# Kernel optimization log

Hardware: AMD Instinct MI355X
Metric: run time of the kernel (lower is better)

The kernel has to match this reference:

```python
import jax, jax.numpy as jnp
import numpy as np

B, N, D = 8, 4096, 256   # batch, nodes, input = hidden = output dim
TD, GD, L = 64, 73, 2    # topo_dim, gdv_dim, num_passes
NEG = -1e9               # fp32 mask value from get_mask_value


def setup_inputs() -> dict:
    key = jax.random.key(0)
    ks = jax.random.split(key, 24)
    s = 0.05
    nrm = lambda k, shp: jax.random.normal(k, shp, jnp.float32) * s
    d = {}
    d['x'] = jax.random.normal(ks[0], (B, N, D), jnp.float32)
    d['adj'] = jax.random.randint(ks[1], (D, D), 0, 2, jnp.int32)
    d['gdv'] = jax.random.uniform(ks[2], (D, GD), dtype=jnp.float32)
    d['W_in'] = nrm(ks[3], (D, D));   d['b_in'] = nrm(ks[4], (D,))
    d['W_out'] = nrm(ks[5], (D, D)); d['b_out'] = nrm(ks[6], (D,))
    d['g1_W'] = nrm(ks[7], (GD, TD));  d['g1_b'] = nrm(ks[8], (TD,))
    d['g2_W'] = nrm(ks[9], (TD, TD));  d['g2_b'] = nrm(ks[10], (TD,))
    d['gres_W'] = nrm(ks[11], (GD, TD)); d['gres_b'] = nrm(ks[12], (TD,))
    d['ln_g'] = jnp.ones((D,), jnp.float32); d['ln_b'] = jnp.zeros((D,), jnp.float32)
    d['Wf'] = nrm(ks[13], (L, D, D)); d['bf'] = nrm(ks[14], (L, D))
    d['Wt'] = nrm(ks[15], (L, TD, D)); d['bt'] = nrm(ks[16], (L, D))
    d['wa_feat'] = nrm(ks[17], (L, 2 * D)); d['ba_feat'] = nrm(ks[18], (L,))
    d['wa_topo'] = nrm(ks[19], (L, 2 * D)); d['ba_topo'] = nrm(ks[20], (L,))
    d['Wo'] = nrm(ks[21], (L, D, D)); d['bo'] = nrm(ks[22], (L, D))
    d['lng'] = jnp.ones((L, D), jnp.float32); d['lnb'] = jnp.zeros((L, D), jnp.float32)
    return d


def _ln(x, g, b, eps=1e-5):
    m = x.mean(-1, keepdims=True)
    v = ((x - m) ** 2).mean(-1, keepdims=True)
    return (x - m) * jax.lax.rsqrt(v + eps) * g + b


def reference(x, adj, gdv, W_in, b_in, W_out, b_out, g1_W, g1_b, g2_W, g2_b,
              gres_W, gres_b, ln_g, ln_b, Wf, bf, Wt, bt, wa_feat, ba_feat,
              wa_topo, ba_topo, Wo, bo, lng, lnb):
    # GDV -> topo embedding; batch-independent, so keep it [D, TD] instead of
    # the original's broadcast [B, D, TD] (same math, no duplicated compute).
    g = gdv / (gdv.sum(1, keepdims=True) + 1e-6)
    t = jax.nn.relu(g @ g1_W + g1_b) @ g2_W + g2_b + (g @ gres_W + gres_b)  # [D, TD]
    mask = adj == 0  # [D, D]
    h = x @ W_in + b_in  # [B, N, D]
    for l in range(L):
        Tp = t @ Wt[l] + bt[l]  # [D, D] topo projection (hidden_dim == D)
        # topo_attn Linear(2D,1) on cat([T_i, T_j]) == (Tp@w_i)_i + (Tp@w_j)_j + bias
        wi, wj = wa_topo[l, :D], wa_topo[l, D:]
        e_topo = jax.nn.leaky_relu((Tp @ wi)[:, None] + (Tp @ wj)[None, :] + ba_topo[l])
        beta = jax.nn.softmax(jnp.where(mask, NEG, e_topo), axis=-1)  # [D, D]
        T_out = beta @ Tp  # [D, D]
        Hp = h @ Wf[l] + bf[l]  # [B, N, D]
        # feature_attn Linear(2D,1) on cat([H_n, T_f]) decomposed the same way
        wh, wt = wa_feat[l, :D], wa_feat[l, D:]
        e_feat = jax.nn.leaky_relu((Hp @ wh)[:, :, None] + (T_out @ wt)[None, None, :] + ba_feat[l])
        alpha = jax.nn.softmax(e_feat, axis=-1)  # [B, N, D]
        h_new = jnp.einsum('bnf,fh->bnh', alpha, T_out)
        # output proj + residual (input==output -> plain add), dropout = identity (eval)
        h = _ln(h_new @ Wo[l] + bo[l] + h, lng[l], lnb[l])
    return _ln(h @ W_out + b_out, ln_g, ln_b)
```

## Files before the change

### kernel.cpp

```cpp
#include <hip/hip_runtime.h>
#include <hip/hip_bf16.h>


typedef float f32x4 __attribute__((ext_vector_type(4)));
typedef short bf16x8 __attribute__((ext_vector_type(8)));

__device__ __forceinline__ unsigned short f2bf(float f) {
  unsigned int u = __builtin_bit_cast(unsigned int, f);
  u += 0x7FFFu + ((u >> 16) & 1u);
  return (unsigned short)(u >> 16);
}
__device__ __forceinline__ float bf2f(unsigned short u) {
  return __builtin_bit_cast(float, (unsigned int)u << 16);
}
__device__ __forceinline__ float lrelu(float x) { return x > 0.f ? x : 0.01f * x; }

template <int CTRL>
__device__ __forceinline__ float dpp_ror_add(float v) {
  int s = __builtin_amdgcn_update_dpp(0, __builtin_bit_cast(int, v), CTRL, 0xf, 0xf, true);
  return v + __builtin_bit_cast(float, s);
}
__device__ __forceinline__ float sum16(float v) {
  v = dpp_ror_add<0x128>(v);
  v = dpp_ror_add<0x124>(v);
  v = dpp_ror_add<0x122>(v);
  v = dpp_ror_add<0x121>(v);
  return v;
}

__device__ __forceinline__ float block_sum(float v, float* s4, int t) {
  v = sum16(v);
  v += __shfl_xor(v, 16, 64);
  v += __shfl_xor(v, 32, 64);
  __syncthreads();
  if ((t & 63) == 0) s4[t >> 6] = v;
  __syncthreads();
  return s4[0] + s4[1] + s4[2] + s4[3];
}
__device__ __forceinline__ float block_max(float v, float* s4, int t) {
#pragma unroll
  for (int m = 1; m < 64; m <<= 1) v = fmaxf(v, __shfl_xor(v, m, 64));
  __syncthreads();
  if ((t & 63) == 0) s4[t >> 6] = v;
  __syncthreads();
  return fmaxf(fmaxf(s4[0], s4[1]), fmaxf(s4[2], s4[3]));
}

__device__ __forceinline__ int swz_off(int k, int n) {
  return ((((k >> 5) * 16 + (n >> 4)) * 4 + ((k >> 3) & 3)) * 16 + (n & 15)) * 8 + (k & 7);
}
__device__ __forceinline__ int alds_byte(int n, int m) {
  int grp = n >> 3;
  int base = (grp * 32 + m) * 16 + (n & 7) * 2;
  return base ^ ((grp & 7) << 4);
}

__global__ void ta_kernel(const float* __restrict__ gdv,
                          const float* __restrict__ g1W, const float* __restrict__ g1b,
                          const float* __restrict__ g2W, const float* __restrict__ g2b,
                          const float* __restrict__ grW, const float* __restrict__ grb,
                          const float* __restrict__ Wt, const float* __restrict__ bt,
                          const float* __restrict__ wat,
                          float* __restrict__ Tp, float* __restrict__ pb, float* __restrict__ qb) {
  int l = blockIdx.x >> 8, i = blockIdx.x & 255, t = threadIdx.x;
  __shared__ float gs[73], as_[64], ts[64], s4[4];
  float gv = (t < 73) ? gdv[i * 73 + t] : 0.f;
  float gsum = block_sum(gv, s4, t);
  if (t < 73) gs[t] = gv / (gsum + 1e-6f);
  __syncthreads();
  if (t < 64) {
    float a = g1b[t], gr = grb[t];
    for (int k = 0; k < 73; ++k) { float gk = gs[k]; a = fmaf(gk, g1W[k * 64 + t], a); gr = fmaf(gk, grW[k * 64 + t], gr); }
    as_[t] = fmaxf(a, 0.f);
    ts[t] = gr + g2b[t];
  }
  __syncthreads();
  float tv = 0.f;
  if (t < 64) {
    tv = ts[t];
    for (int k = 0; k < 64; ++k) tv = fmaf(as_[k], g2W[k * 64 + t], tv);
  }
  __syncthreads();
  if (t < 64) ts[t] = tv;
  __syncthreads();
  float tp = bt[l * 256 + t];
  for (int k = 0; k < 64; ++k) tp = fmaf(ts[k], Wt[(l * 64 + k) * 256 + t], tp);
  Tp[(l * 256 + i) * 256 + t] = tp;
  float pp = block_sum(tp * wat[l * 512 + t], s4, t);
  float qq = block_sum(tp * wat[l * 512 + 256 + t], s4, t);
  if (t == 0) { pb[l * 256 + i] = pp; qb[l * 256 + i] = qq; }
}

__global__ void tb_kernel(const int* __restrict__ adj, const float* __restrict__ Tp,
                          const float* __restrict__ pb, const float* __restrict__ qb,
                          const float* __restrict__ batopo, const float* __restrict__ Wo,
                          const float* __restrict__ wafeat, const float* __restrict__ bafeat,
                          const float* __restrict__ Wf, const float* __restrict__ bfv,
                          const float* __restrict__ Win, const float* __restrict__ Wout,
                          float* __restrict__ rp, float* __restrict__ ub, float* __restrict__ cb,
                          unsigned short* __restrict__ Uws) {
  int b = blockIdx.x, t = threadIdx.x;
  if (b >= 512) {
    int bb = b - 512;
    const float* src = (bb < 16) ? Win : Wout;
    unsigned short* dst = Uws + ((bb < 16) ? 0 : 65536);
    int r0 = (bb & 15) * 16;
    for (int kk = 0; kk < 16; ++kk) {
      int k = r0 + kk;
      dst[swz_off(k, t)] = f2bf(src[k * 256 + t]);
    }
    return;
  }
  int l = b >> 8, i = b & 255;
  __shared__ float beta[256], tout[256], s4[4];
  float e = pb[l * 256 + i] + qb[l * 256 + t] + batopo[l];
  e = lrelu(e);
  if (adj[i * 256 + t] == 0) e = -1e9f;
  float mx = block_max(e, s4, t);
  float w = __expf(e - mx);
  float Z = block_sum(w, s4, t);
  beta[t] = w / Z;
  __syncthreads();
  float acc = 0.f;
  for (int j = 0; j < 256; ++j) acc = fmaf(beta[j], Tp[(l * 256 + j) * 256 + t], acc);
  tout[t] = acc;
  __syncthreads();
  const float* WoL = Wo + l * 65536;
  float macc = 0.f;
  for (int h2 = 0; h2 < 256; ++h2) macc = fmaf(tout[h2], WoL[h2 * 256 + t], macc);
  Uws[131072 + l * 65536 + swz_off(i, t)] = f2bf(macc);
  const float* wf = wafeat + l * 512;
  float rsum = block_sum(tout[t] * wf[256 + t], s4, t);
  if (t == 0) rp[l * 256 + i] = rsum + bafeat[l];
  float usum = block_sum(Wf[(l * 256 + i) * 256 + t] * wf[t], s4, t);
  if (t == 0) ub[l * 256 + i] = usum;
  if (i == 0) {
    float csum = block_sum(bfv[l * 256 + t] * wf[t], s4, t);
    if (t == 0) cb[l] = csum;
  }
}

#define MFMA(A, B, C) __builtin_amdgcn_mfma_f32_16x16x32_bf16(A, B, C, 0, 0, 0)

__device__ __forceinline__ void kloop(const char* smc, const unsigned short* Bws,
                                      int wid, int lane, int li, int g, f32x4 acc[2][2]) {
  const bf16x8* Bw = (const bf16x8*)Bws + wid * 2 * 64 + lane;
  bf16x8 b0 = Bw[0], b1 = Bw[64];
#pragma unroll
  for (int kb = 0; kb < 8; ++kb) {
    bf16x8 nb0, nb1;
    if (kb < 7) {
      nb0 = Bw[(kb + 1) * 1024];
      nb1 = Bw[(kb + 1) * 1024 + 64];
    }
    int grp = kb * 4 + g;
    int ab = ((grp * 32 + li) * 16) ^ ((grp & 7) << 4);
    bf16x8 a0 = *(const bf16x8*)(smc + ab);
    bf16x8 a1 = *(const bf16x8*)(smc + ab + 256);
    acc[0][0] = MFMA(a0, b0, acc[0][0]);
    acc[1][0] = MFMA(a1, b0, acc[1][0]);
    acc[0][1] = MFMA(a0, b1, acc[0][1]);
    acc[1][1] = MFMA(a1, b1, acc[1][1]);
    if (kb < 7) { b0 = nb0; b1 = nb1; }
  }
}

#define S_REDUCE(UBARR, CBV)                                                   \
  {                                                                            \
    float u0_ = UBARR[ncol[0]], u1_ = UBARR[ncol[1]];                          \
    _Pragma("unroll") for (int rt = 0; rt < 2; ++rt) {                         \
      float sp[4];                                                             \
      _Pragma("unroll") for (int r = 0; r < 4; ++r)                            \
        sp[r] = h[rt][0][r] * u0_ + h[rt][1][r] * u1_;                         \
      _Pragma("unroll") for (int r = 0; r < 4; ++r) sp[r] = sum16(sp[r]);      \
      if (li == 0) {                                                           \
        _Pragma("unroll") for (int r = 0; r < 4; ++r)                          \
          red[wid][rt * 16 + g * 4 + r] = sp[r];                               \
      }                                                                        \
    }                                                                          \
    __syncthreads();                                                           \
    if (t < 32) {                                                              \
      float S = 0.f;                                                           \
      _Pragma("unroll") for (int w = 0; w < 8; ++w) S += red[w][t];            \
      row_s[t] = S + (CBV);                                                    \
    }                                                                          \
    __syncthreads();                                                           \
  }

#define LN_STATS()                                                             \
  {                                                                            \
    _Pragma("unroll") for (int rt = 0; rt < 2; ++rt) {                         \
      float sA[4], sQ[4];                                                      \
      _Pragma("unroll") for (int r = 0; r < 4; ++r) {                          \
        float a0 = h[rt][0][r], a1 = h[rt][1][r];                              \
        sA[r] = a0 + a1;                                                       \
        sQ[r] = a0 * a0 + a1 * a1;                                             \
      }                                                                        \
      _Pragma("unroll") for (int r = 0; r < 4; ++r) {                          \
        sA[r] = sum16(sA[r]); sQ[r] = sum16(sQ[r]);                            \
      }                                                                        \
      if (li == 0) {                                                           \
        _Pragma("unroll") for (int r = 0; r < 4; ++r) {                        \
          int row_ = rt * 16 + g * 4 + r;                                      \
          red[wid][row_] = sA[r]; red[8 + wid][row_] = sQ[r];                  \
        }                                                                      \
      }                                                                        \
    }                                                                          \
    __syncthreads();                                                           \
    if (t < 32) {                                                              \
      float S = 0.f, Q = 0.f;                                                  \
      _Pragma("unroll") for (int w = 0; w < 8; ++w) { S += red[w][t]; Q += red[8 + w][t]; } \
      float mean_ = S * (1.f / 256.f);                                         \
      float var_ = Q * (1.f / 256.f) - mean_ * mean_;                          \
      mr_s[t][0] = mean_; mr_s[t][1] = rsqrtf(var_ + 1e-5f);                   \
    }                                                                          \
    __syncthreads();                                                           \
  }

__global__ __launch_bounds__(512) void fused_kernel(
    const float* __restrict__ x,
    const float* __restrict__ rp, const float* __restrict__ ub, const float* __restrict__ cbp,
    const unsigned short* __restrict__ Uws,
    const float* __restrict__ bin, const float* __restrict__ bo,
    const float* __restrict__ lng, const float* __restrict__ lnb,
    const float* __restrict__ bout, const float* __restrict__ lngf, const float* __restrict__ lnbf,
    float* __restrict__ out) {
  __shared__ unsigned short alds[8192];
  __shared__ float c_bin[256], c_bout[256], c_lngf[256], c_lnbf[256];
  __shared__ float c_ub[2][256], c_bo[2][256], c_lng[2][256], c_lnb[2][256], c_rp[2][256];
  __shared__ float red[16][32];
  __shared__ float row_s[32], invz_s[32];
  __shared__ float mr_s[32][2];
  __shared__ float scal_s[4];
  char* smc = (char*)alds;

  const int wg = blockIdx.x, t = threadIdx.x;
  const int wid = t >> 6, lane = t & 63, li = lane & 15, g = lane >> 4;
  const int rowbase = wg * 32;
  int ncol[2]; ncol[0] = wid * 32 + li; ncol[1] = wid * 32 + 16 + li;

  if (t < 256) {
    c_bin[t] = bin[t]; c_ub[0][t] = ub[t]; c_bo[0][t] = bo[t];
    c_lng[0][t] = lng[t]; c_lnb[0][t] = lnb[t]; c_rp[0][t] = rp[t];
  } else {
    int u = t - 256;
    c_bout[u] = bout[u]; c_lngf[u] = lngf[u]; c_lnbf[u] = lnbf[u];
    c_ub[1][u] = ub[256 + u]; c_bo[1][u] = bo[256 + u];
    c_lng[1][u] = lng[256 + u]; c_lnb[1][u] = lnb[256 + u]; c_rp[1][u] = rp[256 + u];
  }
  if (t == 0) { scal_s[2] = cbp[0]; scal_s[3] = cbp[1]; }

#pragma unroll
  for (int it = 0; it < 4; ++it) {
    int flat = it * 2048 + t * 4;
    int m = flat >> 8, col = flat & 255;
    const float4 xv = *(const float4*)(x + (rowbase + m) * 256 + col);
    ushort4 pk; pk.x = f2bf(xv.x); pk.y = f2bf(xv.y); pk.z = f2bf(xv.z); pk.w = f2bf(xv.w);
    *(ushort4*)(smc + alds_byte(col, m)) = pk;
  }
  __syncthreads();
  if (wid < 2) {
    float m2 = fmaxf(fmaxf(c_rp[wid][lane], c_rp[wid][lane + 64]),
                     fmaxf(c_rp[wid][lane + 128], c_rp[wid][lane + 192]));
#pragma unroll
    for (int mm = 1; mm < 64; mm <<= 1) m2 = fmaxf(m2, __shfl_xor(m2, mm, 64));
    if (lane == 0) scal_s[wid] = m2;
  }

  float h[2][2][4];

  {
    f32x4 acc[2][2];
#pragma unroll
    for (int a = 0; a < 2; ++a)
#pragma unroll
      for (int c = 0; c < 2; ++c) { f32x4 z = {0.f, 0.f, 0.f, 0.f}; acc[a][c] = z; }
    kloop(smc, Uws, wid, lane, li, g, acc);
#pragma unroll
    for (int rt = 0; rt < 2; ++rt)
#pragma unroll
      for (int ct = 0; ct < 2; ++ct)
#pragma unroll
        for (int r = 0; r < 4; ++r) h[rt][ct][r] = acc[rt][ct][r] + c_bin[ncol[ct]];
    S_REDUCE(c_ub[0], scal_s[2]);
  }

#pragma unroll 1
  for (int l = 0; l < 2; ++l) {
    {
      int row = t & 31, p = t >> 5;
      float sm = row_s[row];
      float mx = lrelu(sm + scal_s[l]);
      float z = 0.f;
#pragma unroll
      for (int j = 0; j < 2; ++j) {
        int grp = p * 2 + j;
        float w0 = __expf(lrelu(sm + c_rp[l][grp * 8 + 0]) - mx);
        float w1 = __expf(lrelu(sm + c_rp[l][grp * 8 + 1]) - mx);
        float w2 = __expf(lrelu(sm + c_rp[l][grp * 8 + 2]) - mx);
        float w3 = __expf(lrelu(sm + c_rp[l][grp * 8 + 3]) - mx);
        float w4 = __expf(lrelu(sm + c_rp[l][grp * 8 + 4]) - mx);
        float w5 = __expf(lrelu(sm + c_rp[l][grp * 8 + 5]) - mx);
        float w6 = __expf(lrelu(sm + c_rp[l][grp * 8 + 6]) - mx);
        float w7 = __expf(lrelu(sm + c_rp[l][grp * 8 + 7]) - mx);
        unsigned short u0 = f2bf(w0), u1 = f2bf(w1), u2 = f2bf(w2), u3 = f2bf(w3);
        unsigned short u4 = f2bf(w4), u5 = f2bf(w5), u6 = f2bf(w6), u7 = f2bf(w7);
        z += bf2f(u0) + bf2f(u1) + bf2f(u2) + bf2f(u3) +
             bf2f(u4) + bf2f(u5) + bf2f(u6) + bf2f(u7);
        uint4 pk;
        pk.x = (unsigned int)u0 | ((unsigned int)u1 << 16);
        pk.y = (unsigned int)u2 | ((unsigned int)u3 << 16);
        pk.z = (unsigned int)u4 | ((unsigned int)u5 << 16);
        pk.w = (unsigned int)u6 | ((unsigned int)u7 << 16);
        int byte = ((grp * 32 + row) * 16) ^ ((grp & 7) << 4);
        *(uint4*)(smc + byte) = pk;
      }
      red[p][row] = z;
    }
    __syncthreads();
    if (t < 32) {
      float Z = 0.f;
#pragma unroll
      for (int p = 0; p < 16; ++p) Z += red[p][t];
      invz_s[t] = 1.f / Z;
    }
    __syncthreads();

    f32x4 acc[2][2];
#pragma unroll
    for (int a = 0; a < 2; ++a)
#pragma unroll
      for (int c = 0; c < 2; ++c) { f32x4 z = {0.f, 0.f, 0.f, 0.f}; acc[a][c] = z; }
    kloop(smc, Uws + 131072 + l * 65536, wid, lane, li, g, acc);

#pragma unroll
    for (int rt = 0; rt < 2; ++rt)
#pragma unroll
      for (int r = 0; r < 4; ++r) {
        int row = rt * 16 + g * 4 + r;
        float iz = invz_s[row];
#pragma unroll
        for (int ct = 0; ct < 2; ++ct)
          h[rt][ct][r] = fmaf(acc[rt][ct][r], iz, c_bo[l][ncol[ct]] + h[rt][ct][r]);
      }
    LN_STATS();
#pragma unroll
    for (int rt = 0; rt < 2; ++rt)
#pragma unroll
      for (int r = 0; r < 4; ++r) {
        int row = rt * 16 + g * 4 + r;
        float mean = mr_s[row][0], rstd = mr_s[row][1];
#pragma unroll
        for (int ct = 0; ct < 2; ++ct)
          h[rt][ct][r] = (h[rt][ct][r] - mean) * rstd * c_lng[l][ncol[ct]] + c_lnb[l][ncol[ct]];
      }
    if (l == 0) S_REDUCE(c_ub[1], scal_s[3]);
  }

#pragma unroll
  for (int rt = 0; rt < 2; ++rt)
#pragma unroll
    for (int ct = 0; ct < 2; ++ct)
#pragma unroll
      for (int r = 0; r < 4; ++r) {
        int row = rt * 16 + g * 4 + r;
        *(unsigned short*)(smc + alds_byte(ncol[ct], row)) = f2bf(h[rt][ct][r]);
      }
  __syncthreads();
  {
    f32x4 acc[2][2];
#pragma unroll
    for (int a = 0; a < 2; ++a)
#pragma unroll
      for (int c = 0; c < 2; ++c) { f32x4 z = {0.f, 0.f, 0.f, 0.f}; acc[a][c] = z; }
    kloop(smc, Uws + 65536, wid, lane, li, g, acc);
#pragma unroll
    for (int rt = 0; rt < 2; ++rt)
#pragma unroll
      for (int ct = 0; ct < 2; ++ct)
#pragma unroll
        for (int r = 0; r < 4; ++r) h[rt][ct][r] = acc[rt][ct][r] + c_bout[ncol[ct]];
    LN_STATS();
#pragma unroll
    for (int rt = 0; rt < 2; ++rt)
#pragma unroll
      for (int r = 0; r < 4; ++r) {
        int row = rt * 16 + g * 4 + r;
        float mean = mr_s[row][0], rstd = mr_s[row][1];
#pragma unroll
        for (int ct = 0; ct < 2; ++ct)
          out[(rowbase + row) * 256 + ncol[ct]] =
              (h[rt][ct][r] - mean) * rstd * c_lngf[ncol[ct]] + c_lnbf[ncol[ct]];
      }
  }
}

extern "C" void kernel_launch(void* const* d_in, const int* in_sizes, int n_in,
                              void* d_out, int out_size, void* d_ws, size_t ws_size,
                              hipStream_t stream) {
  const float* x    = (const float*)d_in[0];
  const int*   adj  = (const int*)d_in[1];
  const float* gdv  = (const float*)d_in[2];
  const float* Win  = (const float*)d_in[3];
  const float* bin  = (const float*)d_in[4];
  const float* Wout = (const float*)d_in[5];
  const float* bout = (const float*)d_in[6];
  const float* g1W  = (const float*)d_in[7];
  const float* g1b  = (const float*)d_in[8];
  const float* g2W  = (const float*)d_in[9];
  const float* g2b  = (const float*)d_in[10];
  const float* grW  = (const float*)d_in[11];
  const float* grb  = (const float*)d_in[12];
  const float* lngf = (const float*)d_in[13];
  const float* lnbf = (const float*)d_in[14];
  const float* Wf   = (const float*)d_in[15];
  const float* bfv  = (const float*)d_in[16];
  const float* Wt   = (const float*)d_in[17];
  const float* bt   = (const float*)d_in[18];
  const float* waf  = (const float*)d_in[19];
  const float* baf  = (const float*)d_in[20];
  const float* wat  = (const float*)d_in[21];
  const float* bat  = (const float*)d_in[22];
  const float* Wo   = (const float*)d_in[23];
  const float* bo   = (const float*)d_in[24];
  const float* lng  = (const float*)d_in[25];
  const float* lnb  = (const float*)d_in[26];
  float* out = (float*)d_out;

  float* W = (float*)d_ws;
  float* Tp = W;
  float* pb = W + 131072;
  float* qb = W + 131584;
  float* rp = W + 132096;
  float* ub = W + 132608;
  float* cb = W + 133120;
  unsigned short* Uws = (unsigned short*)(W + 133184);

  ta_kernel<<<512, 256, 0, stream>>>(gdv, g1W, g1b, g2W, g2b, grW, grb, Wt, bt, wat, Tp, pb, qb);
  tb_kernel<<<544, 256, 0, stream>>>(adj, Tp, pb, qb, bat, Wo, waf, baf, Wf, bfv, Win, Wout, rp, ub, cb, Uws);
  fused_kernel<<<1024, 512, 0, stream>>>(x, rp, ub, cb, Uws, bin, bo, lng, lnb, bout, lngf, lnbf, out);
}
```

Measured before the change: 75.45 us.

## Deepen B-operand prefetch, raise MFMA priority, stagger workgroup start, nontemporal I/O

```diff
diff --git a/kernel.cpp b/kernel.cpp
--- a/kernel.cpp
+++ b/kernel.cpp
@@ -145,23 +145,27 @@
 __device__ __forceinline__ void kloop(const char* smc, const unsigned short* Bws,
                                       int wid, int lane, int li, int g, f32x4 acc[2][2]) {
   const bf16x8* Bw = (const bf16x8*)Bws + wid * 2 * 64 + lane;
-  bf16x8 b0 = Bw[0], b1 = Bw[64];
+  bf16x8 b0a = Bw[0], b1a = Bw[64];
+  bf16x8 b0b = Bw[1024], b1b = Bw[1024 + 64];
 #pragma unroll
   for (int kb = 0; kb < 8; ++kb) {
     bf16x8 nb0, nb1;
-    if (kb < 7) {
-      nb0 = Bw[(kb + 1) * 1024];
-      nb1 = Bw[(kb + 1) * 1024 + 64];
+    if (kb < 6) {
+      nb0 = Bw[(kb + 2) * 1024];
+      nb1 = Bw[(kb + 2) * 1024 + 64];
     }
     int grp = kb * 4 + g;
     int ab = ((grp * 32 + li) * 16) ^ ((grp & 7) << 4);
     bf16x8 a0 = *(const bf16x8*)(smc + ab);
     bf16x8 a1 = *(const bf16x8*)(smc + ab + 256);
-    acc[0][0] = MFMA(a0, b0, acc[0][0]);
-    acc[1][0] = MFMA(a1, b0, acc[1][0]);
-    acc[0][1] = MFMA(a0, b1, acc[0][1]);
-    acc[1][1] = MFMA(a1, b1, acc[1][1]);
-    if (kb < 7) { b0 = nb0; b1 = nb1; }
+    __builtin_amdgcn_s_setprio(1);
+    acc[0][0] = MFMA(a0, b0a, acc[0][0]);
+    acc[1][0] = MFMA(a1, b0a, acc[1][0]);
+    acc[0][1] = MFMA(a0, b1a, acc[0][1]);
+    acc[1][1] = MFMA(a1, b1a, acc[1][1]);
+    __builtin_amdgcn_s_setprio(0);
+    b0a = b0b; b1a = b1b;
+    if (kb < 6) { b0b = nb0; b1b = nb1; }
   }
 }
 
@@ -239,6 +243,13 @@
   const int rowbase = wg * 32;
   int ncol[2]; ncol[0] = wid * 32 + li; ncol[1] = wid * 32 + 16 + li;
 
+  {
+    int ph = wg & 3;
+    if (ph > 0) __builtin_amdgcn_s_sleep(24);
+    if (ph > 1) __builtin_amdgcn_s_sleep(24);
+    if (ph > 2) __builtin_amdgcn_s_sleep(24);
+  }
+
   if (t < 256) {
     c_bin[t] = bin[t]; c_ub[0][t] = ub[t]; c_bo[0][t] = bo[t];
     c_lng[0][t] = lng[t]; c_lnb[0][t] = lnb[t]; c_rp[0][t] = rp[t];
@@ -254,7 +265,7 @@
   for (int it = 0; it < 4; ++it) {
     int flat = it * 2048 + t * 4;
     int m = flat >> 8, col = flat & 255;
-    const float4 xv = *(const float4*)(x + (rowbase + m) * 256 + col);
+    const f32x4 xv = __builtin_nontemporal_load((const f32x4*)(x + (rowbase + m) * 256 + col));
     ushort4 pk; pk.x = f2bf(xv.x); pk.y = f2bf(xv.y); pk.z = f2bf(xv.z); pk.w = f2bf(xv.w);
     *(ushort4*)(smc + alds_byte(col, m)) = pk;
   }
@@ -388,9 +399,10 @@
         int row = rt * 16 + g * 4 + r;
         float mean = mr_s[row][0], rstd = mr_s[row][1];
 #pragma unroll
-        for (int ct = 0; ct < 2; ++ct)
-          out[(rowbase + row) * 256 + ncol[ct]] =
-              (h[rt][ct][r] - mean) * rstd * c_lngf[ncol[ct]] + c_lnbf[ncol[ct]];
+        for (int ct = 0; ct < 2; ++ct) {
+          float v = (h[rt][ct][r] - mean) * rstd * c_lngf[ncol[ct]] + c_lnbf[ncol[ct]];
+          __builtin_nontemporal_store(v, out + (rowbase + row) * 256 + ncol[ct]);
+        }
       }
   }
 }
```

Result: faster. 69.57 us (-7.8%).

## Restructure fused kernel: fewer barriers, prefetched B tiles, packed bf16 converts

Applied to the files above, without the earlier changes.

```diff
diff --git a/kernel.cpp b/kernel.cpp
--- a/kernel.cpp
+++ b/kernel.cpp
@@ -5,13 +5,17 @@
 typedef float f32x4 __attribute__((ext_vector_type(4)));
 typedef short bf16x8 __attribute__((ext_vector_type(8)));
 
+__device__ __forceinline__ unsigned int cvt_pk(float lo, float hi) {
+  unsigned int r;
+  asm("v_cvt_pk_bf16_f32 %0, %1, %2" : "=v"(r) : "v"(lo), "v"(hi));
+  return r;
+}
+__device__ __forceinline__ float bfl(unsigned int p) { return __builtin_bit_cast(float, p << 16); }
+__device__ __forceinline__ float bfh(unsigned int p) { return __builtin_bit_cast(float, p & 0xFFFF0000u); }
 __device__ __forceinline__ unsigned short f2bf(float f) {
   unsigned int u = __builtin_bit_cast(unsigned int, f);
   u += 0x7FFFu + ((u >> 16) & 1u);
   return (unsigned short)(u >> 16);
-}
-__device__ __forceinline__ float bf2f(unsigned short u) {
-  return __builtin_bit_cast(float, (unsigned int)u << 16);
 }
 __device__ __forceinline__ float lrelu(float x) { return x > 0.f ? x : 0.01f * x; }
 
@@ -142,79 +146,99 @@
 
 #define MFMA(A, B, C) __builtin_amdgcn_mfma_f32_16x16x32_bf16(A, B, C, 0, 0, 0)
 
+__device__ __forceinline__ void preB(const unsigned short* Bws, int wid, int lane,
+                                     bf16x8& p0, bf16x8& p1) {
+  const bf16x8* Bw = (const bf16x8*)Bws + wid * 2 * 64 + lane;
+  p0 = Bw[0]; p1 = Bw[64];
+}
+
 __device__ __forceinline__ void kloop(const char* smc, const unsigned short* Bws,
-                                      int wid, int lane, int li, int g, f32x4 acc[2][2]) {
+                                      int wid, int lane, int li, int g,
+                                      bf16x8 b0, bf16x8 b1, f32x4 acc[2][2]) {
   const bf16x8* Bw = (const bf16x8*)Bws + wid * 2 * 64 + lane;
-  bf16x8 b0 = Bw[0], b1 = Bw[64];
 #pragma unroll
   for (int kb = 0; kb < 8; ++kb) {
     bf16x8 nb0, nb1;
-    if (kb < 7) {
-      nb0 = Bw[(kb + 1) * 1024];
-      nb1 = Bw[(kb + 1) * 1024 + 64];
-    }
+    if (kb < 7) { nb0 = Bw[(kb + 1) * 1024]; nb1 = Bw[(kb + 1) * 1024 + 64]; }
     int grp = kb * 4 + g;
     int ab = ((grp * 32 + li) * 16) ^ ((grp & 7) << 4);
     bf16x8 a0 = *(const bf16x8*)(smc + ab);
     bf16x8 a1 = *(const bf16x8*)(smc + ab + 256);
+    __builtin_amdgcn_s_setprio(1);
     acc[0][0] = MFMA(a0, b0, acc[0][0]);
     acc[1][0] = MFMA(a1, b0, acc[1][0]);
     acc[0][1] = MFMA(a0, b1, acc[0][1]);
     acc[1][1] = MFMA(a1, b1, acc[1][1]);
+    __builtin_amdgcn_s_setprio(0);
     if (kb < 7) { b0 = nb0; b1 = nb1; }
   }
 }
 
-#define S_REDUCE(UBARR, CBV)                                                   \
-  {                                                                            \
-    float u0_ = UBARR[ncol[0]], u1_ = UBARR[ncol[1]];                          \
-    _Pragma("unroll") for (int rt = 0; rt < 2; ++rt) {                         \
-      float sp[4];                                                             \
-      _Pragma("unroll") for (int r = 0; r < 4; ++r)                            \
-        sp[r] = h[rt][0][r] * u0_ + h[rt][1][r] * u1_;                         \
-      _Pragma("unroll") for (int r = 0; r < 4; ++r) sp[r] = sum16(sp[r]);      \
-      if (li == 0) {                                                           \
-        _Pragma("unroll") for (int r = 0; r < 4; ++r)                          \
-          red[wid][rt * 16 + g * 4 + r] = sp[r];                               \
-      }                                                                        \
-    }                                                                          \
-    __syncthreads();                                                           \
-    if (t < 32) {                                                              \
-      float S = 0.f;                                                           \
-      _Pragma("unroll") for (int w = 0; w < 8; ++w) S += red[w][t];            \
-      row_s[t] = S + (CBV);                                                    \
-    }                                                                          \
-    __syncthreads();                                                           \
-  }
-
-#define LN_STATS()                                                             \
-  {                                                                            \
-    _Pragma("unroll") for (int rt = 0; rt < 2; ++rt) {                         \
-      float sA[4], sQ[4];                                                      \
+__device__ __forceinline__ float comb8(const float* p) {
+  f32x4 a = *(const f32x4*)p;
+  f32x4 b = *(const f32x4*)(p + 4);
+  return ((a.x + a.y) + (a.z + a.w)) + ((b.x + b.y) + (b.z + b.w));
+}
+
+#define ACC_INIT(acc)                                                          \
+  _Pragma("unroll") for (int a_ = 0; a_ < 2; ++a_)                             \
+    _Pragma("unroll") for (int c_ = 0; c_ < 2; ++c_) {                         \
+      f32x4 z_ = {0.f, 0.f, 0.f, 0.f}; acc[a_][c_] = z_; }
+
+#define LN_PART(WITHG, GU0, GU1)                                               \
+  { _Pragma("unroll") for (int rt = 0; rt < 2; ++rt) {                         \
+      float sA[4], sQ[4], sG[4];                                               \
       _Pragma("unroll") for (int r = 0; r < 4; ++r) {                          \
         float a0 = h[rt][0][r], a1 = h[rt][1][r];                              \
-        sA[r] = a0 + a1;                                                       \
-        sQ[r] = a0 * a0 + a1 * a1;                                             \
+        sA[r] = a0 + a1; sQ[r] = fmaf(a0, a0, a1 * a1);                        \
+        sG[r] = (WITHG) ? fmaf(a0, (GU0), a1 * (GU1)) : 0.f;                   \
       }                                                                        \
       _Pragma("unroll") for (int r = 0; r < 4; ++r) {                          \
         sA[r] = sum16(sA[r]); sQ[r] = sum16(sQ[r]);                            \
+        if (WITHG) sG[r] = sum16(sG[r]);                                       \
       }                                                                        \
       if (li == 0) {                                                           \
         _Pragma("unroll") for (int r = 0; r < 4; ++r) {                        \
           int row_ = rt * 16 + g * 4 + r;                                      \
-          red[wid][row_] = sA[r]; red[8 + wid][row_] = sQ[r];                  \
+          red2[row_][wid] = sA[r]; red2[row_][8 + wid] = sQ[r];                \
+          if (WITHG) red2[row_][16 + wid] = sG[r];                             \
         }                                                                      \
       }                                                                        \
+    } }
+
+#define LN_APPLY(LNGA, LNBA)                                                   \
+  { _Pragma("unroll") for (int rt = 0; rt < 2; ++rt)                           \
+      _Pragma("unroll") for (int r = 0; r < 4; ++r) {                          \
+        int row_ = rt * 16 + g * 4 + r;                                        \
+        float S_ = comb8(&red2[row_][0]), Q_ = comb8(&red2[row_][8]);          \
+        float mean_ = S_ * (1.f / 256.f);                                      \
+        float rstd_ = rsqrtf(Q_ * (1.f / 256.f) - mean_ * mean_ + 1e-5f);      \
+        _Pragma("unroll") for (int ct = 0; ct < 2; ++ct)                       \
+          h[rt][ct][r] = (h[rt][ct][r] - mean_) * rstd_ * LNGA[ncol[ct]] + LNBA[ncol[ct]]; \
+      } }
+
+#define ALPHA_GEN(LIDX, SM_EXPR)                                               \
+  { int arow_ = wid * 4 + g;                                                   \
+    float sm = (SM_EXPR);                                                      \
+    float mx = lrelu(sm + scal_s[LIDX]);                                       \
+    float z = 0.f;                                                             \
+    _Pragma("unroll") for (int half = 0; half < 2; ++half) {                   \
+      int grp = li * 2 + half;                                                 \
+      float w_[8];                                                             \
+      _Pragma("unroll") for (int j = 0; j < 8; ++j) {                          \
+        float rv = c_rp_t[LIDX][(half * 8 + j) * 16 + li];                     \
+        w_[j] = __expf(lrelu(sm + rv) - mx);                                   \
+      }                                                                        \
+      uint4 pk;                                                                \
+      pk.x = cvt_pk(w_[0], w_[1]); pk.y = cvt_pk(w_[2], w_[3]);                \
+      pk.z = cvt_pk(w_[4], w_[5]); pk.w = cvt_pk(w_[6], w_[7]);                \
+      z += bfl(pk.x) + bfh(pk.x) + bfl(pk.y) + bfh(pk.y) +                     \
+           bfl(pk.z) + bfh(pk.z) + bfl(pk.w) + bfh(pk.w);                      \
+      int byte_ = ((grp * 32 + arow_) * 16) ^ ((grp & 7) << 4);                \
+      *(uint4*)(smc + byte_) = pk;                                             \
     }                                                                          \
-    __syncthreads();                                                           \
-    if (t < 32) {                                                              \
-      float S = 0.f, Q = 0.f;                                                  \
-      _Pragma("unroll") for (int w = 0; w < 8; ++w) { S += red[w][t]; Q += red[8 + w][t]; } \
-      float mean_ = S * (1.f / 256.f);                                         \
-      float var_ = Q * (1.f / 256.f) - mean_ * mean_;                          \
-      mr_s[t][0] = mean_; mr_s[t][1] = rsqrtf(var_ + 1e-5f);                   \
-    }                                                                          \
-    __syncthreads();                                                           \
+    z = sum16(z);                                                              \
+    if (li == 0) invz_s[arow_] = 1.f / z;                                      \
   }
 
 __global__ __launch_bounds__(512) void fused_kernel(
@@ -227,11 +251,12 @@
     float* __restrict__ out) {
   __shared__ unsigned short alds[8192];
   __shared__ float c_bin[256], c_bout[256], c_lngf[256], c_lnbf[256];
-  __shared__ float c_ub[2][256], c_bo[2][256], c_lng[2][256], c_lnb[2][256], c_rp[2][256];
-  __shared__ float red[16][32];
-  __shared__ float row_s[32], invz_s[32];
-  __shared__ float mr_s[32][2];
-  __shared__ float scal_s[4];
+  __shared__ float c_ub[2][256], c_bo[2][256], c_lng[2][256], c_lnb[2][256];
+  __shared__ float c_rp_t[2][256];
+  __shared__ float c_gu[256];
+  __shared__ float red2[32][24];
+  __shared__ float invz_s[32];
+  __shared__ float scal_s[8];
   char* smc = (char*)alds;
 
   const int wg = blockIdx.x, t = threadIdx.x;
@@ -239,14 +264,26 @@
   const int rowbase = wg * 32;
   int ncol[2]; ncol[0] = wid * 32 + li; ncol[1] = wid * 32 + 16 + li;
 
+  {
+    int ph = (wg >> 8) & 3;
+    if (ph > 0) __builtin_amdgcn_s_sleep(39);
+    if (ph > 1) __builtin_amdgcn_s_sleep(39);
+    if (ph > 2) __builtin_amdgcn_s_sleep(39);
+  }
+
+  bf16x8 pb0, pb1;
+  preB(Uws, wid, lane, pb0, pb1);
+
   if (t < 256) {
     c_bin[t] = bin[t]; c_ub[0][t] = ub[t]; c_bo[0][t] = bo[t];
-    c_lng[0][t] = lng[t]; c_lnb[0][t] = lnb[t]; c_rp[0][t] = rp[t];
+    c_lng[0][t] = lng[t]; c_lnb[0][t] = lnb[t];
+    c_rp_t[0][(t & 15) * 16 + (t >> 4)] = rp[t];
   } else {
     int u = t - 256;
     c_bout[u] = bout[u]; c_lngf[u] = lngf[u]; c_lnbf[u] = lnbf[u];
     c_ub[1][u] = ub[256 + u]; c_bo[1][u] = bo[256 + u];
-    c_lng[1][u] = lng[256 + u]; c_lnb[1][u] = lnb[256 + u]; c_rp[1][u] = rp[256 + u];
+    c_lng[1][u] = lng[256 + u]; c_lnb[1][u] = lnb[256 + u];
+    c_rp_t[1][(u & 15) * 16 + (u >> 4)] = rp[256 + u];
   }
   if (t == 0) { scal_s[2] = cbp[0]; scal_s[3] = cbp[1]; }
 
@@ -254,145 +291,152 @@
   for (int it = 0; it < 4; ++it) {
     int flat = it * 2048 + t * 4;
     int m = flat >> 8, col = flat & 255;
-    const float4 xv = *(const float4*)(x + (rowbase + m) * 256 + col);
-    ushort4 pk; pk.x = f2bf(xv.x); pk.y = f2bf(xv.y); pk.z = f2bf(xv.z); pk.w = f2bf(xv.w);
-    *(ushort4*)(smc + alds_byte(col, m)) = pk;
-  }
-  __syncthreads();
+    const f32x4 xv = __builtin_nontemporal_load((const f32x4*)(x + (rowbase + m) * 256 + col));
+    uint2 pk; pk.x = cvt_pk(xv.x, xv.y); pk.y = cvt_pk(xv.z, xv.w);
+    *(uint2*)(smc + alds_byte(col, m)) = pk;
+  }
+  __syncthreads();
+
   if (wid < 2) {
-    float m2 = fmaxf(fmaxf(c_rp[wid][lane], c_rp[wid][lane + 64]),
-                     fmaxf(c_rp[wid][lane + 128], c_rp[wid][lane + 192]));
+    float m2 = fmaxf(fmaxf(c_rp_t[wid][lane], c_rp_t[wid][lane + 64]),
+                     fmaxf(c_rp_t[wid][lane + 128], c_rp_t[wid][lane + 192]));
 #pragma unroll
     for (int mm = 1; mm < 64; mm <<= 1) m2 = fmaxf(m2, __shfl_xor(m2, mm, 64));
     if (lane == 0) scal_s[wid] = m2;
+  } else if (wid == 2) {
+    float ga = 0.f, ba = 0.f;
+#pragma unroll
+    for (int j = 0; j < 4; ++j) {
+      int idx = lane * 4 + j;
+      float u1v = c_ub[1][idx];
+      float gvv = c_lng[0][idx] * u1v;
+      c_gu[idx] = gvv;
+      ga += gvv;
+      ba = fmaf(c_lnb[0][idx], u1v, ba);
+    }
+    ga = sum16(ga); ga += __shfl_xor(ga, 16, 64); ga += __shfl_xor(ga, 32, 64);
+    ba = sum16(ba); ba += __shfl_xor(ba, 16, 64); ba += __shfl_xor(ba, 32, 64);
+    if (lane == 0) { scal_s[4] = ga; scal_s[5] = ba + cbp[1]; }
   }
 
   float h[2][2][4];
 
   {
-    f32x4 acc[2][2];
-#pragma unroll
-    for (int a = 0; a < 2; ++a)
-#pragma unroll
-      for (int c = 0; c < 2; ++c) { f32x4 z = {0.f, 0.f, 0.f, 0.f}; acc[a][c] = z; }
-    kloop(smc, Uws, wid, lane, li, g, acc);
+    f32x4 acc[2][2]; ACC_INIT(acc);
+    kloop(smc, Uws, wid, lane, li, g, pb0, pb1, acc);
 #pragma unroll
     for (int rt = 0; rt < 2; ++rt)
 #pragma unroll
       for (int ct = 0; ct < 2; ++ct)
 #pragma unroll
         for (int r = 0; r < 4; ++r) h[rt][ct][r] = acc[rt][ct][r] + c_bin[ncol[ct]];
-    S_REDUCE(c_ub[0], scal_s[2]);
-  }
-
-#pragma unroll 1
-  for (int l = 0; l < 2; ++l) {
-    {
-      int row = t & 31, p = t >> 5;
-      float sm = row_s[row];
-      float mx = lrelu(sm + scal_s[l]);
-      float z = 0.f;
-#pragma unroll
-      for (int j = 0; j < 2; ++j) {
-        int grp = p * 2 + j;
-        float w0 = __expf(lrelu(sm + c_rp[l][grp * 8 + 0]) - mx);
-        float w1 = __expf(lrelu(sm + c_rp[l][grp * 8 + 1]) - mx);
-        float w2 = __expf(lrelu(sm + c_rp[l][grp * 8 + 2]) - mx);
-        float w3 = __expf(lrelu(sm + c_rp[l][grp * 8 + 3]) - mx);
-        float w4 = __expf(lrelu(sm + c_rp[l][grp * 8 + 4]) - mx);
-        float w5 = __expf(lrelu(sm + c_rp[l][grp * 8 + 5]) - mx);
-        float w6 = __expf(lrelu(sm + c_rp[l][grp * 8 + 6]) - mx);
-        float w7 = __expf(lrelu(sm + c_rp[l][grp * 8 + 7]) - mx);
-        unsigned short u0 = f2bf(w0), u1 = f2bf(w1), u2 = f2bf(w2), u3 = f2bf(w3);
-        unsigned short u4 = f2bf(w4), u5 = f2bf(w5), u6 = f2bf(w6), u7 = f2bf(w7);
-        z += bf2f(u0) + bf2f(u1) + bf2f(u2) + bf2f(u3) +
-             bf2f(u4) + bf2f(u5) + bf2f(u6) + bf2f(u7);
-        uint4 pk;
-        pk.x = (unsigned int)u0 | ((unsigned int)u1 << 16);
-        pk.y = (unsigned int)u2 | ((unsigned int)u3 << 16);
-        pk.z = (unsigned int)u4 | ((unsigned int)u5 << 16);
-        pk.w = (unsigned int)u6 | ((unsigned int)u7 << 16);
-        int byte = ((grp * 32 + row) * 16) ^ ((grp & 7) << 4);
-        *(uint4*)(smc + byte) = pk;
+    float u0_ = c_ub[0][ncol[0]], u1_ = c_ub[0][ncol[1]];
+#pragma unroll
+    for (int rt = 0; rt < 2; ++rt) {
+      float sp[4];
+#pragma unroll
+      for (int r = 0; r < 4; ++r) sp[r] = h[rt][0][r] * u0_ + h[rt][1][r] * u1_;
+#pragma unroll
+      for (int r = 0; r < 4; ++r) sp[r] = sum16(sp[r]);
+      if (li == 0) {
+#pragma unroll
+        for (int r = 0; r < 4; ++r) red2[rt * 16 + g * 4 + r][wid] = sp[r];
       }
-      red[p][row] = z;
     }
-    __syncthreads();
-    if (t < 32) {
-      float Z = 0.f;
-#pragma unroll
-      for (int p = 0; p < 16; ++p) Z += red[p][t];
-      invz_s[t] = 1.f / Z;
+  }
+  preB(Uws + 131072, wid, lane, pb0, pb1);
+  __syncthreads();
+
+  ALPHA_GEN(0, comb8(&red2[wid * 4 + g][0]) + scal_s[2]);
+  __syncthreads();
+
+  {
+    f32x4 acc[2][2]; ACC_INIT(acc);
+    kloop(smc, Uws + 131072, wid, lane, li, g, pb0, pb1, acc);
+#pragma unroll
+    for (int rt = 0; rt < 2; ++rt)
+#pragma unroll
+      for (int r = 0; r < 4; ++r) {
+        int row_ = rt * 16 + g * 4 + r;
+        float iz = invz_s[row_];
+#pragma unroll
+        for (int ct = 0; ct < 2; ++ct)
+          h[rt][ct][r] = fmaf(acc[rt][ct][r], iz, c_bo[0][ncol[ct]] + h[rt][ct][r]);
+      }
+    float gu0 = c_gu[ncol[0]], gu1 = c_gu[ncol[1]];
+    LN_PART(true, gu0, gu1);
+  }
+  preB(Uws + 131072 + 65536, wid, lane, pb0, pb1);
+  __syncthreads();
+
+  LN_APPLY(c_lng[0], c_lnb[0]);
+  {
+    int arw = wid * 4 + g;
+    float S_ = comb8(&red2[arw][0]), Q_ = comb8(&red2[arw][8]), G_ = comb8(&red2[arw][16]);
+    float mean_ = S_ * (1.f / 256.f);
+    float rstd_ = rsqrtf(Q_ * (1.f / 256.f) - mean_ * mean_ + 1e-5f);
+    float sm1 = rstd_ * (G_ - mean_ * scal_s[4]) + scal_s[5];
+    ALPHA_GEN(1, sm1);
+  }
+  __syncthreads();
+
+  {
+    f32x4 acc[2][2]; ACC_INIT(acc);
+    kloop(smc, Uws + 131072 + 65536, wid, lane, li, g, pb0, pb1, acc);
+#pragma unroll
+    for (int rt = 0; rt < 2; ++rt)
+#pragma unroll
+      for (int r = 0; r < 4; ++r) {
+        int row_ = rt * 16 + g * 4 + r;
+        float iz = invz_s[row_];
+#pragma unroll
+        for (int ct = 0; ct < 2; ++ct)
+          h[rt][ct][r] = fmaf(acc[rt][ct][r], iz, c_bo[1][ncol[ct]] + h[rt][ct][r]);
+      }
+    LN_PART(false, 0.f, 0.f);
+  }
+  preB(Uws + 65536, wid, lane, pb0, pb1);
+  __syncthreads();
+
+  LN_APPLY(c_lng[1], c_lnb[1]);
+#pragma unroll
+  for (int rt = 0; rt < 2; ++rt)
+#pragma unroll
+    for (int r = 0; r < 4; ++r) {
+      int row_ = rt * 16 + g * 4 + r;
+      unsigned int p = cvt_pk(h[rt][0][r], h[rt][1][r]);
+      *(unsigned short*)(smc + alds_byte(ncol[0], row_)) = (unsigned short)p;
+      *(unsigned short*)(smc + alds_byte(ncol[1], row_)) = (unsigned short)(p >> 16);
     }
-    __syncthreads();
-
-    f32x4 acc[2][2];
-#pragma unroll
-    for (int a = 0; a < 2; ++a)
-#pragma unroll
-      for (int c = 0; c < 2; ++c) { f32x4 z = {0.f, 0.f, 0.f, 0.f}; acc[a][c] = z; }
-    kloop(smc, Uws + 131072 + l * 65536, wid, lane, li, g, acc);
-
+  __syncthreads();
+
+  {
+    f32x4 acc[2][2]; ACC_INIT(acc);
+    kloop(smc, Uws + 65536, wid, lane, li, g, pb0, pb1, acc);
 #pragma unroll
     for (int rt = 0; rt < 2; ++rt)
 #pragma unroll
-      for (int r = 0; r < 4; ++r) {
-        int row = rt * 16 + g * 4 + r;
-        float iz = invz_s[row];
-#pragma unroll
-        for (int ct = 0; ct < 2; ++ct)
-          h[rt][ct][r] = fmaf(acc[rt][ct][r], iz, c_bo[l][ncol[ct]] + h[rt][ct][r]);
+      for (int ct = 0; ct < 2; ++ct)
+#pragma unroll
+        for (int r = 0; r < 4; ++r) h[rt][ct][r] = acc[rt][ct][r] + c_bout[ncol[ct]];
+    LN_PART(false, 0.f, 0.f);
+  }
+  __syncthreads();
+
+#pragma unroll
+  for (int rt = 0; rt < 2; ++rt)
+#pragma unroll
+    for (int r = 0; r < 4; ++r) {
+      int row_ = rt * 16 + g * 4 + r;
+      float S_ = comb8(&red2[row_][0]), Q_ = comb8(&red2[row_][8]);
+      float mean_ = S_ * (1.f / 256.f);
+      float rstd_ = rsqrtf(Q_ * (1.f / 256.f) - mean_ * mean_ + 1e-5f);
+#pragma unroll
+      for (int ct = 0; ct < 2; ++ct) {
+        float v = (h[rt][ct][r] - mean_) * rstd_ * c_lngf[ncol[ct]] + c_lnbf[ncol[ct]];
+        __builtin_nontemporal_store(v, out + (rowbase + row_) * 256 + ncol[ct]);
       }
-    LN_STATS();
-#pragma unroll
-    for (int rt = 0; rt < 2; ++rt)
-#pragma unroll
-      for (int r = 0; r < 4; ++r) {
-        int row = rt * 16 + g * 4 + r;
-        float mean = mr_s[row][0], rstd = mr_s[row][1];
-#pragma unroll
-        for (int ct = 0; ct < 2; ++ct)
-          h[rt][ct][r] = (h[rt][ct][r] - mean) * rstd * c_lng[l][ncol[ct]] + c_lnb[l][ncol[ct]];
-      }
-    if (l == 0) S_REDUCE(c_ub[1], scal_s[3]);
-  }
-
-#pragma unroll
-  for (int rt = 0; rt < 2; ++rt)
-#pragma unroll
-    for (int ct = 0; ct < 2; ++ct)
-#pragma unroll
-      for (int r = 0; r < 4; ++r) {
-        int row = rt * 16 + g * 4 + r;
-        *(unsigned short*)(smc + alds_byte(ncol[ct], row)) = f2bf(h[rt][ct][r]);
-      }
-  __syncthreads();
-  {
-    f32x4 acc[2][2];
-#pragma unroll
-    for (int a = 0; a < 2; ++a)
-#pragma unroll
-      for (int c = 0; c < 2; ++c) { f32x4 z = {0.f, 0.f, 0.f, 0.f}; acc[a][c] = z; }
-    kloop(smc, Uws + 65536, wid, lane, li, g, acc);
-#pragma unroll
-    for (int rt = 0; rt < 2; ++rt)
-#pragma unroll
-      for (int ct = 0; ct < 2; ++ct)
-#pragma unroll
-        for (int r = 0; r < 4; ++r) h[rt][ct][r] = acc[rt][ct][r] + c_bout[ncol[ct]];
-    LN_STATS();
-#pragma unroll
-    for (int rt = 0; rt < 2; ++rt)
-#pragma unroll
-      for (int r = 0; r < 4; ++r) {
-        int row = rt * 16 + g * 4 + r;
-        float mean = mr_s[row][0], rstd = mr_s[row][1];
-#pragma unroll
-        for (int ct = 0; ct < 2; ++ct)
-          out[(rowbase + row) * 256 + ncol[ct]] =
-              (h[rt][ct][r] - mean) * rstd * c_lngf[ncol[ct]] + c_lnbf[ncol[ct]];
-      }
-  }
+    }
 }
 
 extern "C" void kernel_launch(void* const* d_in, const int* in_sizes, int n_in,
```

Result: slower. 92.97 us (+23.2%).
